# Optimization experiments

Measured on AMD Instinct MI355X. Metric: run time of the kernel, lower is better.

Reference implementation:

```python
import jax, jax.numpy as jnp
import numpy as np

N = 4096
DIM = 128      # dim_in
HID = 256      # mlp hidden_dim
K_IN = 8       # k for linear_k

def _knn_edges(dist, k):
    # dist: [n,n]; k nearest neighbors excluding self (matches heapq loop)
    n = dist.shape[0]
    d = jnp.where(jnp.eye(n, dtype=bool), jnp.inf, dist)
    nbr = jax.lax.top_k(-d, k)[1]                     # [n,k] indices of k smallest
    src = jnp.repeat(jnp.arange(n), k)                # res[0] = i
    dst = nbr.reshape(-1)                             # res[1] = neighbor
    return src, dst

def _gcn_conv(x, src, dst, W, b):
    # torch_geometric GCNConv: add self loops + symmetric normalization
    n = x.shape[0]
    loop = jnp.arange(n)
    s = jnp.concatenate([src, loop])
    t = jnp.concatenate([dst, loop])
    xw = x @ W
    deg = jax.ops.segment_sum(jnp.ones(s.shape[0], x.dtype), t, num_segments=n)
    dinv = jax.lax.rsqrt(deg)                         # deg >= 1 due to self loops
    norm = dinv[s] * dinv[t]
    out = jax.ops.segment_sum(norm[:, None] * xw[s], t, num_segments=n)
    return out + b

def _gcn(x, src, dst, Wg1, bg1, Wg2, bg2):
    h = jax.nn.relu(_gcn_conv(x, src, dst, Wg1, bg1))
    h = _gcn_conv(h, src, dst, Wg2, bg2)              # dropout is identity in eval
    return jax.nn.log_softmax(h, axis=1)

def _conv2d(x, w, b):
    y = jax.lax.conv_general_dilated(x, w, (1, 1), 'SAME',
        dimension_numbers=('NCHW', 'OIHW', 'NCHW'))
    return y + b.reshape(1, -1, 1, 1)

def setup_inputs():
    key = jax.random.key(0)
    ks = jax.random.split(key, 20)
    f32 = jnp.float32
    def w(k, shape):
        fan = shape[0]
        return (jax.random.uniform(k, shape, f32) * 2 - 1) * (1.0 / np.sqrt(fan))
    return {
        'data_x_1': jax.random.normal(ks[0], (1, N, 4), f32),
        'data_x_2': jax.random.normal(ks[1], (1, N, K_IN, 4), f32),
        'Wk': w(ks[2], (K_IN, 1)),        'bk': jnp.zeros((1,), f32),
        'Wg1': w(ks[3], (8, DIM // 2)),   'bg1': jnp.zeros((DIM // 2,), f32),
        'Wg2': w(ks[4], (DIM // 2, DIM)), 'bg2': jnp.zeros((DIM,), f32),
        'Wq': w(ks[5], (3 * DIM, DIM)),   'bq': jnp.zeros((DIM,), f32),
        'Wkey': w(ks[6], (3 * DIM, DIM)), 'bkey': jnp.zeros((DIM,), f32),
        'Woff': w(ks[7], (4, DIM)),       'boff': jnp.zeros((DIM,), f32),
        'pw': jnp.full((1,), 0.25, f32),
        'Wf1': w(ks[8], (DIM, HID)),      'bf1': jnp.zeros((HID,), f32),
        'Wf2': w(ks[9], (HID, HID)),      'bf2': jnp.zeros((HID,), f32),
        'Wf3': w(ks[10], (HID, 4)),       'bf3': jnp.zeros((4,), f32),
        'Wcy3': w(ks[11], (1, 1, 1, 3)),  'bcy3': jnp.zeros((1,), f32),
        'Wcx3': w(ks[12], (1, 1, 3, 1)),  'bcx3': jnp.zeros((1,), f32),
        'Wcy5': w(ks[13], (1, 1, 1, 5)),  'bcy5': jnp.zeros((1,), f32),
        'Wcx5': w(ks[14], (1, 1, 5, 1)),  'bcx5': jnp.zeros((1,), f32),
        'Wcy9': w(ks[15], (1, 1, 1, 9)),  'bcy9': jnp.zeros((1,), f32),
        'Wcx9': w(ks[16], (1, 1, 9, 1)),  'bcx9': jnp.zeros((1,), f32),
    }

def reference(data_x_1, data_x_2, Wk, bk, Wg1, bg1, Wg2, bg2, Wq, bq, Wkey, bkey,
              Woff, boff, pw, Wf1, bf1, Wf2, bf2, Wf3, bf3,
              Wcy3, bcy3, Wcx3, bcx3, Wcy5, bcy5, Wcx5, bcx5, Wcy9, bcy9, Wcx9, bcx9):
    # linear_k over k dimension: [1,n,k,4] -> transpose -> [1,n,4,k] -> [1,n,4]
    dx2 = jnp.swapaxes(data_x_2, 2, 3)
    dx2_out = (dx2 @ Wk + bk)[..., 0]
    data_x = jnp.concatenate([data_x_1, dx2_out], axis=2)   # [1,n,8]
    Ot = data_x[:, :, 4:]                                   # [1,n,4]

    pos = data_x[:, :, 0:2]
    diff = pos[:, :, None, :] - pos[:, None, :, :]          # [1,n,n,2]
    distances = jnp.linalg.norm(diff, axis=3)               # [1,n,n]
    maxd = jnp.max(distances, axis=2, keepdims=True)
    oushi_atte = 1.0 - distances / maxd                     # [1,n,n]

    x0 = data_x[0]
    dist0 = jax.lax.stop_gradient(distances[0])             # knn on detached dist
    embs = []
    for kk in (3, 5, 9):
        src, dst = _knn_edges(dist0, kk)
        embs.append(_gcn(x0, src, dst, Wg1, bg1, Wg2, bg2)[None])
    embedding = jnp.concatenate(embs, axis=2)               # [1,n,3*DIM]

    query = embedding @ Wq + bq                             # [1,n,DIM]
    key_t = embedding @ Wkey + bkey
    scores = jnp.einsum('bnd,bmd->bnm', query, key_t) / jnp.sqrt(jnp.float32(DIM))
    A = scores / jnp.max(scores, axis=2, keepdims=True)     # [1,n,n]

    A4 = A[None]                                            # [1,1,n,n]
    c3 = _conv2d(A4, Wcy3, bcy3) + _conv2d(A4, Wcx3, bcx3)
    c5 = _conv2d(A4, Wcy5, bcy5) + _conv2d(A4, Wcx5, bcx5)
    c9 = _conv2d(A4, Wcy9, bcy9) + _conv2d(A4, Wcx9, bcx9)

    A_cat = jnp.concatenate([A, oushi_atte, c3[0], c5[0], c9[0]], axis=2)  # [1,n,5n]
    A_cat = (A_cat - A_cat.min()) / (A_cat.max() - A_cat.min())

    Ot5 = jnp.tile(Ot, (1, 5, 1))                           # [1,5n,4]
    h = jnp.matmul(A_cat, Ot5)                              # [1,n,4]
    h = h @ Woff + boff                                     # [1,n,DIM]
    h = jnp.where(h > 0, h, pw * h)                         # PReLU (scalar weight)
    h = jax.nn.relu(h @ Wf1 + bf1)
    h = jax.nn.relu(h @ Wf2 + bf2)
    return h @ Wf3 + bf3                                    # [1,n,4]
```

## Files before the change

### kernel.cpp

```cpp
#include <hip/hip_runtime.h>
#include <math.h>

#define NN 4096

typedef __bf16 bf16x8 __attribute__((ext_vector_type(8)));
typedef float  f32x4  __attribute__((ext_vector_type(4)));
typedef _Float16 half4 __attribute__((ext_vector_type(4)));

static __device__ __forceinline__ unsigned enc_f(float f){
    unsigned u = __float_as_uint(f);
    return (u & 0x80000000u) ? ~u : (u | 0x80000000u);
}
static __device__ __forceinline__ float dec_f(unsigned u){
    unsigned b = (u & 0x80000000u) ? (u & 0x7fffffffu) : ~u;
    return __uint_as_float(b);
}
static __device__ __forceinline__ float4 shfl4(float4 v, int src){
    float4 r;
    r.x = __shfl(v.x, src, 64);
    r.y = __shfl(v.y, src, 64);
    r.z = __shfl(v.z, src, 64);
    r.w = __shfl(v.w, src, 64);
    return r;
}
static __device__ __forceinline__ unsigned long long shflx_u64(unsigned long long v, int m){
    unsigned lo = __shfl_xor((unsigned)(v & 0xffffffffu), m, 64);
    unsigned hi = __shfl_xor((unsigned)(v >> 32), m, 64);
    return ((unsigned long long)hi << 32) | lo;
}

__global__ void k_prep(const float* __restrict__ dx1, const float* __restrict__ dx2,
                       const float* __restrict__ Wk, const float* __restrict__ bk,
                       float* __restrict__ x0, float* __restrict__ colsum,
                       float2* __restrict__ pos, float4* __restrict__ otp){
    int n = blockIdx.x*blockDim.x + threadIdx.x;
    if (n >= NN) return;
    float wk[8];
    #pragma unroll
    for (int j=0;j<8;j++) wk[j] = Wk[j];
    float bkv = bk[0];
    float4 d1 = *(const float4*)&dx1[n*4];
    pos[n] = make_float2(d1.x, d1.y);
    #pragma unroll
    for (int c=0;c<4;c++) x0[n*8+c] = (&d1.x)[c];
    float4 ot;
    #pragma unroll
    for (int c=0;c<4;c++){
        float acc = bkv;
        #pragma unroll
        for (int j=0;j<8;j++) acc += dx2[(n*8+j)*4+c]*wk[j];
        x0[n*8+4+c] = acc;
        (&ot.x)[c] = acc;
        atomicAdd(&colsum[c], acc);
    }
    otp[n] = ot;
}

__global__ void k_ty(const float* __restrict__ x0,
        const float* __restrict__ Wcy3, const float* __restrict__ Wcy5, const float* __restrict__ Wcy9,
        float* __restrict__ Ty){
    int j = blockIdx.x*256 + threadIdx.x;
    if (j >= NN) return;
    float Cy[9];
    #pragma unroll
    for (int o=-4;o<=4;o++){
        float c = Wcy9[o+4];
        if (o>=-2 && o<=2) c += Wcy5[o+2];
        if (o>=-1 && o<=1) c += Wcy3[o+1];
        Cy[o+4] = c;
    }
    float4 acc = {0,0,0,0};
    #pragma unroll
    for (int o=-4;o<=4;o++){
        int jj = j - o;
        if ((unsigned)jj < NN){
            float4 ot = *(const float4*)&x0[jj*8+4];
            float c = Cy[o+4];
            acc.x += c*ot.x; acc.y += c*ot.y; acc.z += c*ot.z; acc.w += c*ot.w;
        }
    }
    *(float4*)&Ty[j*4] = acc;
}

#define KCAP 192
__global__ __launch_bounds__(256) void k_dist(const float2* __restrict__ pos,
        const float4* __restrict__ otp,
        float* __restrict__ maxd, int* __restrict__ nbr,
        int* __restrict__ cnt3, int* __restrict__ cnt5, int* __restrict__ cnt9,
        float* __restrict__ dOt){
    __shared__ unsigned long long cbuf[4][KCAP];
    int tid = threadIdx.x;
    int w = tid >> 6, lane = tid & 63;
    int i = blockIdx.x*4 + w;
    float2 pi = pos[i];

    float lmax = 0.f, lmin = INFINITY;
    float4 dacc = {0,0,0,0};
    for (int t=0;t<64;t++){
        int j = (t<<6) | lane;
        float2 p = pos[j];
        float dx = pi.x - p.x, dy = pi.y - p.y;
        float d = sqrtf(dx*dx + dy*dy);
        lmax = fmaxf(lmax, d);
        float4 otj = otp[j];
        dacc.x += d*otj.x; dacc.y += d*otj.y; dacc.z += d*otj.z; dacc.w += d*otj.w;
        if (j != i) lmin = fminf(lmin, d);
    }
    #pragma unroll
    for (int m=1;m<64;m<<=1){
        lmax = fmaxf(lmax, __shfl_xor(lmax, m, 64));
        dacc.x += __shfl_xor(dacc.x, m, 64);
        dacc.y += __shfl_xor(dacc.y, m, 64);
        dacc.z += __shfl_xor(dacc.z, m, 64);
        dacc.w += __shfl_xor(dacc.w, m, 64);
    }
    if (lane==0){
        maxd[i] = lmax;
        *(float4*)&dOt[i*4] = dacc;
    }
    float v = lmin, T = 0.f;
    #pragma unroll
    for (int r=0;r<9;r++){
        float m = v;
        #pragma unroll
        for (int s=1;s<64;s<<=1) m = fminf(m, __shfl_xor(m, s, 64));
        T = m;
        if (v == m) v = INFINITY;
    }

    int base = 0;
    for (int t=0;t<64;t++){
        int j = (t<<6) | lane;
        float2 p = pos[j];
        float dx = pi.x - p.x, dy = pi.y - p.y;
        float d = sqrtf(dx*dx + dy*dy);
        bool pass = (j != i) && (d <= T);
        unsigned long long b = __ballot(pass);
        if (b){
            int pre = __popcll(b & ((1ull<<lane)-1ull));
            int idx = base + pre;
            if (pass && idx < KCAP)
                cbuf[w][idx] = ((unsigned long long)__float_as_uint(d) << 32) | (unsigned)j;
            base += __popcll(b);
        }
    }
    int M = base < KCAP ? base : KCAP;

    unsigned long long c0 = (lane      < M) ? cbuf[w][lane]      : ~0ULL;
    unsigned long long c1 = (lane+64   < M) ? cbuf[w][lane+64]   : ~0ULL;
    unsigned long long c2 = (lane+128  < M) ? cbuf[w][lane+128]  : ~0ULL;
    for (int r=0;r<9;r++){
        unsigned long long mv = c0 < c1 ? c0 : c1;
        mv = mv < c2 ? mv : c2;
        #pragma unroll
        for (int s=1;s<64;s<<=1){
            unsigned long long o = shflx_u64(mv, s);
            if (o < mv) mv = o;
        }
        if (c0 == mv) c0 = ~0ULL;
        else if (c1 == mv) c1 = ~0ULL;
        else if (c2 == mv) c2 = ~0ULL;
        if (lane == 0){
            int j = (int)(mv & 0xffffffffu);
            nbr[i*9+r] = j;
            atomicAdd(&cnt9[j], 1);
            if (r<5) atomicAdd(&cnt5[j], 1);
            if (r<3) atomicAdd(&cnt3[j], 1);
        }
    }
}

__global__ __launch_bounds__(256) void k_scan(const int* __restrict__ cnt3,
        const int* __restrict__ cnt5, const int* __restrict__ cnt9,
        int* __restrict__ offc, float* __restrict__ dinvc){
    __shared__ int part[256];
    int tid = threadIdx.x;
    for (int g=0; g<3; g++){
        const int* cp = g==0?cnt3:(g==1?cnt5:cnt9);
        int base = tid*16;
        int loc[16]; int s=0;
        #pragma unroll
        for (int q=0;q<16;q++){ loc[q]=s; s += cp[base+q]; }
        part[tid]=s; __syncthreads();
        for (int d=1; d<256; d<<=1){
            int v = (tid>=d) ? part[tid-d] : 0;
            __syncthreads();
            part[tid] += v;
            __syncthreads();
        }
        int pre = (tid==0) ? 0 : part[tid-1];
        #pragma unroll
        for (int q=0;q<16;q++){
            offc[g*NN + base + q]  = pre + loc[q];
            dinvc[g*NN + base + q] = rsqrtf((float)cp[base+q] + 1.f);
        }
        __syncthreads();
    }
}

__global__ void k_fill(const int* __restrict__ nbr, const int* __restrict__ offc,
        int* __restrict__ cur, int* __restrict__ rev){
    int i = blockIdx.x*256 + threadIdx.x;
    if (i >= NN) return;
    #pragma unroll
    for (int t=0;t<9;t++){
        int j = nbr[i*9+t];
        int gmin = t<3 ? 0 : (t<5 ? 1 : 2);
        for (int g=gmin; g<3; g++){
            int pos = atomicAdd(&cur[g*NN+j], 1);
            int rb = (g==0) ? 0 : (g==1 ? NN*3 : NN*8);
            rev[rb + offc[g*NN+j] + pos] = i;
        }
    }
}

__global__ void k_y1(const float* __restrict__ x0, const float* __restrict__ Wg1,
                     float* __restrict__ xw){
    int idx = blockIdx.x*256 + threadIdx.x;
    if (idx >= NN*64) return;
    int n = idx>>6, c = idx&63;
    float acc = 0.f;
    #pragma unroll
    for (int k=0;k<8;k++) acc += x0[n*8+k]*Wg1[k*64+c];
    xw[idx] = acc;
}

__global__ __launch_bounds__(256) void k_h1y2(const float* __restrict__ xw,
        const int* __restrict__ offc,
        const int* __restrict__ cnt3, const int* __restrict__ cnt5, const int* __restrict__ cnt9,
        const int* __restrict__ rev, const float* __restrict__ dinvc,
        const float* __restrict__ bg1, const float* __restrict__ Wg2,
        float* __restrict__ y2){
    __shared__ float h1s[12][64];
    int n0 = blockIdx.x*4, tid = threadIdx.x;
    for (int s=tid; s<768; s+=256){
        int p = s>>6, k = s&63, g = p>>2, n = n0+(p&3);
        const int* cp = g==0?cnt3:(g==1?cnt5:cnt9);
        int rb = (g==0) ? 0 : (g==1 ? NN*3 : NN*8);
        int cnt = cp[n];
        int o = rb + offc[g*NN+n];
        float dv = dinvc[g*NN+n];
        float srow = dv*xw[n*64+k];
        for (int e=0;e<cnt;e++){
            int i = rev[o+e];
            srow += dinvc[g*NN+i]*xw[i*64+k];
        }
        float v = dv*srow + bg1[k];
        h1s[p][k] = v>0.f ? v : 0.f;
    }
    __syncthreads();
    int c = tid & 127, ph = tid>>7;
    float a6[6] = {0,0,0,0,0,0};
    for (int k=0;k<64;k++){
        float w = Wg2[k*128+c];
        #pragma unroll
        for (int q=0;q<6;q++) a6[q] += h1s[q*2+ph][k]*w;
    }
    #pragma unroll
    for (int q=0;q<6;q++){
        int p = q*2+ph, g = p>>2, n = n0+(p&3);
        float dv = dinvc[g*NN+n];
        y2[(size_t)g*NN*128 + (size_t)n*128 + c] = dv*a6[q];
    }
}

__global__ __launch_bounds__(128) void k_fin(const float* __restrict__ y2,
        const int* __restrict__ offc,
        const int* __restrict__ cnt3, const int* __restrict__ cnt5, const int* __restrict__ cnt9,
        const int* __restrict__ rev, const float* __restrict__ dinvc,
        const float* __restrict__ bg2, float* __restrict__ emb){
    __shared__ float sm[2], ss[2];
    int b = blockIdx.x;
    int n = b & (NN-1), g = b >> 12;
    const int* cp = g==0?cnt3:(g==1?cnt5:cnt9);
    int rb = (g==0) ? 0 : (g==1 ? NN*3 : NN*8);
    int cnt = cp[n];
    int o = rb + offc[g*NN+n];
    float dv = dinvc[g*NN+n];
    int c = threadIdx.x;
    const float* yg = y2 + (size_t)g*NN*128;
    float s = yg[(size_t)n*128 + c];
    for (int e=0;e<cnt;e++){
        int i = rev[o+e];
        s += yg[(size_t)i*128 + c];
    }
    float v = dv*s + bg2[c];
    float m = v;
    #pragma unroll
    for (int st=1;st<64;st<<=1) m = fmaxf(m, __shfl_xor(m, st, 64));
    if ((c&63)==0) sm[c>>6] = m;
    __syncthreads();
    m = fmaxf(sm[0], sm[1]);
    float e = expf(v - m);
    float t = e;
    #pragma unroll
    for (int st=1;st<64;st<<=1) t += __shfl_xor(t, st, 64);
    if ((c&63)==0) ss[c>>6] = t;
    __syncthreads();
    t = ss[0]+ss[1];
    emb[n*384 + g*128 + c] = v - m - logf(t);
}

__global__ __launch_bounds__(256) void k_qk(const float* __restrict__ emb,
        const float* __restrict__ Wq, const float* __restrict__ bq,
        const float* __restrict__ Wkey, const float* __restrict__ bkey,
        __bf16* __restrict__ qh, __bf16* __restrict__ ql,
        __bf16* __restrict__ kh, __bf16* __restrict__ kl){
    __shared__ float es[8][384];
    int n0 = blockIdx.x*8;
    int tid = threadIdx.x;
    for (int idx=tid; idx<8*384; idx+=256){
        int m = idx/384, k = idx%384;
        es[m][k] = emb[(n0+m)*384+k];
    }
    __syncthreads();
    int c = tid & 127;
    int sel = tid >> 7;
    const float* W = sel ? Wkey : Wq;
    float b = sel ? bkey[c] : bq[c];
    float acc[8];
    #pragma unroll
    for (int m=0;m<8;m++) acc[m]=b;
    for (int k=0;k<384;k++){
        float w = W[k*128+c];
        #pragma unroll
        for (int m=0;m<8;m++) acc[m] += es[m][k]*w;
    }
    __bf16* oh = sel ? kh : qh;
    __bf16* ol = sel ? kl : ql;
    #pragma unroll
    for (int m=0;m<8;m++){
        float v = acc[m];
        __bf16 h = (__bf16)v;
        oh[(size_t)(n0+m)*128+c] = h;
        ol[(size_t)(n0+m)*128+c] = (__bf16)(v - (float)h);
    }
}

__global__ __launch_bounds__(256) void k_scores(
        const __bf16* __restrict__ qh, const __bf16* __restrict__ ql,
        const __bf16* __restrict__ kh, const __bf16* __restrict__ kl,
        _Float16* __restrict__ scores,
        unsigned* __restrict__ rowmaxenc, unsigned* __restrict__ rowminenc){
    __shared__ float tl[4][16][68];
    int bx = blockIdx.x & 31;
    int by = blockIdx.x >> 5;
    int tid = threadIdx.x;
    int w = tid >> 6, lane = tid & 63;
    int li = lane & 15, g = lane >> 4;
    int r0 = by*128 + (w>>1)*64;
    int c0 = bx*128 + (w&1)*64;

    f32x4 acc[4][4] = {};
    for (int ks=0; ks<4; ++ks){
        int kofs = ks*32 + g*8;
        bf16x8 ah[4], al[4], bh[4], bl[4];
        #pragma unroll
        for (int f=0; f<4; ++f){
            ah[f] = *(const bf16x8*)&qh[(size_t)(r0+f*16+li)*128 + kofs];
            al[f] = *(const bf16x8*)&ql[(size_t)(r0+f*16+li)*128 + kofs];
            bh[f] = *(const bf16x8*)&kh[(size_t)(c0+f*16+li)*128 + kofs];
            bl[f] = *(const bf16x8*)&kl[(size_t)(c0+f*16+li)*128 + kofs];
        }
        #pragma unroll
        for (int fr=0; fr<4; ++fr){
            #pragma unroll
            for (int fc=0; fc<4; ++fc){
                acc[fr][fc] = __builtin_amdgcn_mfma_f32_16x16x32_bf16(ah[fr], bh[fc], acc[fr][fc], 0, 0, 0);
                acc[fr][fc] = __builtin_amdgcn_mfma_f32_16x16x32_bf16(ah[fr], bl[fc], acc[fr][fc], 0, 0, 0);
                acc[fr][fc] = __builtin_amdgcn_mfma_f32_16x16x32_bf16(al[fr], bh[fc], acc[fr][fc], 0, 0, 0);
            }
        }
    }
    #pragma unroll
    for (int fr=0; fr<4; ++fr){
        #pragma unroll
        for (int r=0; r<4; ++r){
            int row = r0 + fr*16 + g*4 + r;
            float mx = -INFINITY, mn = INFINITY;
            #pragma unroll
            for (int fc=0; fc<4; ++fc){
                float v = acc[fr][fc][r];
                mx = fmaxf(mx, v);
                mn = fminf(mn, v);
            }
            #pragma unroll
            for (int s=1; s<16; s<<=1){
                mx = fmaxf(mx, __shfl_xor(mx, s, 64));
                mn = fminf(mn, __shfl_xor(mn, s, 64));
            }
            if (li == 0){
                atomicMax(&rowmaxenc[row], enc_f(mx));
                atomicMin(&rowminenc[row], enc_f(mn));
            }
        }
    }
    for (int fr=0; fr<4; ++fr){
        #pragma unroll
        for (int fc=0; fc<4; ++fc)
            #pragma unroll
            for (int r=0; r<4; ++r)
                tl[w][g*4+r][fc*16+li] = acc[fr][fc][r];
        __syncthreads();
        #pragma unroll
        for (int q=0; q<4; ++q){
            int row = q*4 + g;
            float4 v;
            v.x = tl[w][row][li*4+0];
            v.y = tl[w][row][li*4+1];
            v.z = tl[w][row][li*4+2];
            v.w = tl[w][row][li*4+3];
            half4 hv = { (_Float16)v.x, (_Float16)v.y, (_Float16)v.z, (_Float16)v.w };
            *(half4*)&scores[(size_t)(r0+fr*16+row)*NN + c0 + li*4] = hv;
        }
        __syncthreads();
    }
}

__global__ void k_invr(const unsigned* __restrict__ rowmaxenc, float* __restrict__ invr){
    int i = blockIdx.x*256 + threadIdx.x;
    if (i >= NN) return;
    invr[i] = 1.f/dec_f(rowmaxenc[i]);
}

__global__ __launch_bounds__(256) void k_cconv(const _Float16* __restrict__ scores,
        const float* __restrict__ invr,
        const float* __restrict__ Wcy3, const float* __restrict__ Wcx3,
        const float* __restrict__ Wcy5, const float* __restrict__ Wcx5,
        const float* __restrict__ Wcy9, const float* __restrict__ Wcx9,
        const float* __restrict__ bcy3, const float* __restrict__ bcx3,
        const float* __restrict__ bcy5, const float* __restrict__ bcx5,
        const float* __restrict__ bcy9, const float* __restrict__ bcx9,
        float* __restrict__ mnmx){
    __shared__ float smn[4], smx[4];
    int tid = threadIdx.x;
    int w = tid >> 6, lane = tid & 63;
    int strip = blockIdx.x;
    int i0 = (blockIdx.y*4 + w)*19;
    int colbase = strip*248 - 4 + lane*4;
    bool lv = (colbase >= 0) && (colbase + 3 < NN);
    bool outLane = (lane >= 1) && (lane < 63) && lv;

    float wy3[3],wx3[3],wy5[5],wx5[5],wy9[9],wx9[9];
    #pragma unroll
    for (int t=0;t<3;t++){ wy3[t]=Wcy3[t]; wx3[t]=Wcx3[t]; }
    #pragma unroll
    for (int t=0;t<5;t++){ wy5[t]=Wcy5[t]; wx5[t]=Wcx5[t]; }
    #pragma unroll
    for (int t=0;t<9;t++){ wy9[t]=Wcy9[t]; wx9[t]=Wcx9[t]; }
    float bc3 = bcy3[0]+bcx3[0];
    float bc5 = bcy5[0]+bcx5[0];
    float bc9 = bcy9[0]+bcx9[0];

    float4 win[9];
    float mn = INFINITY, mx = -INFINITY;
    const int laneL = lane - 1, laneR = lane + 1;

    for (int tb = 0; tb < 3; ++tb){
        #pragma unroll
        for (int u = 0; u < 9; ++u){
            int t  = tb*9 + u;
            int ri = i0 - 4 + t;
            float4 a = make_float4(0,0,0,0);
            if (((unsigned)ri < NN) && lv){
                float iv = invr[ri];
                half4 hv = *(const half4*)&scores[(size_t)ri*NN + colbase];
                a.x = (float)hv.x*iv; a.y = (float)hv.y*iv;
                a.z = (float)hv.z*iv; a.w = (float)hv.w*iv;
            }
            win[u] = a;
            int ro = i0 + t - 8;
            if (t >= 8 && ro < NN){
                float4 ctr = win[(u+5)%9];
                float4 wl = shfl4(ctr, laneL);
                float4 wr = shfl4(ctr, laneR);
                if (outLane){
                    float cw[12] = {wl.x,wl.y,wl.z,wl.w, ctr.x,ctr.y,ctr.z,ctr.w, wr.x,wr.y,wr.z,wr.w};
                    #pragma unroll
                    for (int c=0;c<4;c++){
                        float cx9 = ((win[(u+1)%9][c]*wx9[0] + win[(u+2)%9][c]*wx9[1]) + (win[(u+3)%9][c]*wx9[2] + win[(u+4)%9][c]*wx9[3]))
                                  + ((win[(u+5)%9][c]*wx9[4] + win[(u+6)%9][c]*wx9[5]) + (win[(u+7)%9][c]*wx9[6] + win[(u+8)%9][c]*wx9[7]))
                                  + win[u][c]*wx9[8];
                        float cx5 = ((win[(u+3)%9][c]*wx5[0] + win[(u+4)%9][c]*wx5[1]) + (win[(u+5)%9][c]*wx5[2] + win[(u+6)%9][c]*wx5[3]))
                                  + win[(u+7)%9][c]*wx5[4];
                        float cx3 = (win[(u+4)%9][c]*wx3[0] + win[(u+5)%9][c]*wx3[1]) + win[(u+6)%9][c]*wx3[2];
                        float cy9 = ((cw[c+0]*wy9[0] + cw[c+1]*wy9[1]) + (cw[c+2]*wy9[2] + cw[c+3]*wy9[3]))
                                  + ((cw[c+4]*wy9[4] + cw[c+5]*wy9[5]) + (cw[c+6]*wy9[6] + cw[c+7]*wy9[7]))
                                  + cw[c+8]*wy9[8];
                        float cy5 = ((cw[c+2]*wy5[0] + cw[c+3]*wy5[1]) + (cw[c+4]*wy5[2] + cw[c+5]*wy5[3]))
                                  + cw[c+6]*wy5[4];
                        float cy3 = (cw[c+3]*wy3[0] + cw[c+4]*wy3[1]) + cw[c+5]*wy3[2];
                        float c3v = cy3+cx3+bc3, c5v = cy5+cx5+bc5, c9v = cy9+cx9+bc9;
                        mn = fminf(mn, fminf(fminf(c3v,c5v),c9v));
                        mx = fmaxf(mx, fmaxf(fmaxf(c3v,c5v),c9v));
                    }
                }
            }
        }
    }
    #pragma unroll
    for (int m=1; m<64; m<<=1){
        mn = fminf(mn, __shfl_xor(mn, m, 64));
        mx = fmaxf(mx, __shfl_xor(mx, m, 64));
    }
    if (lane == 0){ smn[w] = mn; smx[w] = mx; }
    __syncthreads();
    if (tid == 0){
        float a0 = fminf(fminf(smn[0],smn[1]), fminf(smn[2],smn[3]));
        float b0 = fmaxf(fmaxf(smx[0],smx[1]), fmaxf(smx[2],smx[3]));
        int bid = blockIdx.y*gridDim.x + blockIdx.x;
        mnmx[bid] = a0;
        mnmx[1024 + bid] = b0;
    }
}

__global__ __launch_bounds__(256) void k_kot(const __bf16* __restrict__ kh, const __bf16* __restrict__ kl,
        const float* __restrict__ x0, const float* __restrict__ Ty,
        float* __restrict__ kOt){
    __shared__ float red[256][8];
    int d = blockIdx.x, tid = threadIdx.x;
    float a[8] = {0,0,0,0,0,0,0,0};
    for (int j = tid; j < NN; j += 256){
        float kv = (float)kh[(size_t)j*128 + d] + (float)kl[(size_t)j*128 + d];
        float4 ot = *(const float4*)&x0[j*8+4];
        float4 ty = *(const float4*)&Ty[j*4];
        a[0] += kv*ot.x; a[1] += kv*ot.y; a[2] += kv*ot.z; a[3] += kv*ot.w;
        a[4] += kv*ty.x; a[5] += kv*ty.y; a[6] += kv*ty.z; a[7] += kv*ty.w;
    }
    #pragma unroll
    for (int q=0;q<8;q++) red[tid][q] = a[q];
    __syncthreads();
    for (int s=128; s>0; s>>=1){
        if (tid < s){
            #pragma unroll
            for (int q=0;q<8;q++) red[tid][q] += red[tid+s][q];
        }
        __syncthreads();
    }
    if (tid < 8) kOt[d*8 + tid] = red[0][tid];
}

__global__ __launch_bounds__(256) void k_asd(
        const __bf16* __restrict__ qh, const __bf16* __restrict__ ql,
        const float* __restrict__ kOt,
        const unsigned* __restrict__ rowmaxenc, const float* __restrict__ maxd,
        const float* __restrict__ dOt, const float* __restrict__ colsum,
        const float* __restrict__ bcy3, const float* __restrict__ bcx3,
        const float* __restrict__ bcy5, const float* __restrict__ bcx5,
        const float* __restrict__ bcy9, const float* __restrict__ bcx9,
        float* __restrict__ ASdot, float* __restrict__ Bv){
    __shared__ float kst[128*8];
    int tid = threadIdx.x;
    for (int s = tid; s < 1024; s += 256) kst[s] = kOt[s];
    __syncthreads();
    int lane = tid & 63, r = tid >> 6;
    int i = blockIdx.x*4 + r;
    float a[8] = {0,0,0,0,0,0,0,0};
    #pragma unroll
    for (int dd=0; dd<2; ++dd){
        int d = lane + dd*64;
        float qv = (float)qh[(size_t)i*128 + d] + (float)ql[(size_t)i*128 + d];
        #pragma unroll
        for (int q=0;q<8;q++) a[q] += qv * kst[d*8+q];
    }
    #pragma unroll
    for (int m=1; m<64; m<<=1){
        #pragma unroll
        for (int q=0;q<8;q++) a[q] += __shfl_xor(a[q], m, 64);
    }
    if (lane == 0){
        float iv = 1.f/dec_f(rowmaxenc[i]);
        float imv = 1.f/maxd[i];
        float bcsum = bcy3[0]+bcx3[0]+bcy5[0]+bcx5[0]+bcy9[0]+bcx9[0];
        float k = 1.f + bcsum;
        float4 cs = *(const float4*)colsum;
        float4 dv = *(const float4*)&dOt[i*4];
        float4 pa = {iv*a[0], iv*a[1], iv*a[2], iv*a[3]};
        float4 b;
        b.x = cs.x*k - imv*dv.x + iv*a[4];
        b.y = cs.y*k - imv*dv.y + iv*a[5];
        b.z = cs.z*k - imv*dv.z + iv*a[6];
        b.w = cs.w*k - imv*dv.w + iv*a[7];
        *(float4*)&ASdot[i*4] = pa;
        *(float4*)&Bv[i*4]    = b;
    }
}

__global__ __launch_bounds__(256) void k_gmm(const float* __restrict__ mnmx,
        const unsigned* __restrict__ rowminenc, const unsigned* __restrict__ rowmaxenc,
        float* __restrict__ gmm){
    __shared__ float smn[256], smx[256];
    int tid = threadIdx.x;
    float mn = 0.f, mx = 1.f;
    for (int i=tid; i<NN; i+=256){
        float rmx = dec_f(rowmaxenc[i]);
        float q = dec_f(rowminenc[i]) / rmx;
        mn = fminf(mn, fminf(1.f, q));
        mx = fmaxf(mx, fmaxf(1.f, q));
    }
    for (int b=tid; b<918; b+=256){
        mn = fminf(mn, mnmx[b]);
        mx = fmaxf(mx, mnmx[1024+b]);
    }
    smn[tid]=mn; smx[tid]=mx; __syncthreads();
    for (int s=128;s>0;s>>=1){
        if (tid<s){ smn[tid]=fminf(smn[tid],smn[tid+s]); smx[tid]=fmaxf(smx[tid],smx[tid+s]); }
        __syncthreads();
    }
    if (tid==0){ gmm[0]=smn[0]; gmm[1]=smx[0]; }
}

__global__ void k_hfin(const float* __restrict__ ASdot, const float* __restrict__ Bv,
        const float* __restrict__ Wcx3, const float* __restrict__ Wcx5, const float* __restrict__ Wcx9,
        const float* __restrict__ gmm, const float* __restrict__ colsum,
        float* __restrict__ hfin){
    int i = blockIdx.x*256 + threadIdx.x;
    if (i >= NN) return;
    float Cx[9];
    #pragma unroll
    for (int o=-4;o<=4;o++){
        float c = Wcx9[o+4];
        if (o>=-2 && o<=2) c += Wcx5[o+2];
        if (o>=-1 && o<=1) c += Wcx3[o+1];
        Cx[o+4] = c;
    }
    float4 h = *(const float4*)&Bv[i*4];
    float4 a0 = *(const float4*)&ASdot[i*4];
    h.x += a0.x; h.y += a0.y; h.z += a0.z; h.w += a0.w;
    #pragma unroll
    for (int o=-4;o<=4;o++){
        int r = i + o;
        if ((unsigned)r < NN){
            float4 av = *(const float4*)&ASdot[r*4];
            float c = Cx[o+4];
            h.x += c*av.x; h.y += c*av.y; h.z += c*av.z; h.w += c*av.w;
        }
    }
    float mnv = gmm[0], mxv = gmm[1];
    float s = 1.f/(mxv-mnv), oa = -mnv*s;
    float4 cs = *(const float4*)colsum;
    float4 out;
    out.x = s*h.x + 5.f*oa*cs.x;
    out.y = s*h.y + 5.f*oa*cs.y;
    out.z = s*h.z + 5.f*oa*cs.z;
    out.w = s*h.w + 5.f*oa*cs.w;
    *(float4*)&hfin[i*4] = out;
}

__global__ __launch_bounds__(256) void k_mlp(const float* __restrict__ hfin,
        const float* __restrict__ Woff, const float* __restrict__ boff, const float* __restrict__ pw,
        const float* __restrict__ Wf1, const float* __restrict__ bf1,
        const float* __restrict__ Wf2, const float* __restrict__ bf2,
        const float* __restrict__ Wf3, const float* __restrict__ bf3,
        float* __restrict__ out){
    __shared__ float h1[8][128];
    __shared__ float h2[8][256];
    __shared__ float h3[8][256];
    int n0 = blockIdx.x*8, tid = threadIdx.x;
    float p = pw[0];
    {
        int c = tid & 127, mb = (tid>>7)*4;
        #pragma unroll
        for (int mm=0; mm<4; mm++){
            int m = mb+mm;
            float v = boff[c];
            #pragma unroll
            for (int k=0;k<4;k++) v += hfin[(n0+m)*4+k]*Woff[k*128+c];
            h1[m][c] = v>0.f ? v : p*v;
        }
    }
    __syncthreads();
    {
        int c = tid;
        float acc[8];
        #pragma unroll
        for (int m=0;m<8;m++) acc[m] = bf1[c];
        for (int k=0;k<128;k++){
            float w = Wf1[k*256+c];
            #pragma unroll
            for (int m=0;m<8;m++) acc[m] += h1[m][k]*w;
        }
        #pragma unroll
        for (int m=0;m<8;m++) h2[m][c] = acc[m]>0.f?acc[m]:0.f;
    }
    __syncthreads();
    {
        int c = tid;
        float acc[8];
        #pragma unroll
        for (int m=0;m<8;m++) acc[m] = bf2[c];
        for (int k=0;k<256;k++){
            float w = Wf2[k*256+c];
            #pragma unroll
            for (int m=0;m<8;m++) acc[m] += h2[m][k]*w;
        }
        #pragma unroll
        for (int m=0;m<8;m++) h3[m][c] = acc[m]>0.f?acc[m]:0.f;
    }
    __syncthreads();
    int w = tid >> 6, lane = tid & 63;
    #pragma unroll
    for (int mm=0; mm<2; ++mm){
        int m = w*2 + mm;
        float4 acc = {0,0,0,0};
        #pragma unroll
        for (int q=0;q<4;q++){
            int k = lane + q*64;
            float hv = h3[m][k];
            float4 w3 = *(const float4*)&Wf3[k*4];
            acc.x += hv*w3.x; acc.y += hv*w3.y; acc.z += hv*w3.z; acc.w += hv*w3.w;
        }
        #pragma unroll
        for (int s=1; s<64; s<<=1){
            acc.x += __shfl_xor(acc.x, s, 64);
            acc.y += __shfl_xor(acc.y, s, 64);
            acc.z += __shfl_xor(acc.z, s, 64);
            acc.w += __shfl_xor(acc.w, s, 64);
        }
        if (lane == 0){
            float4 o;
            o.x = acc.x + bf3[0]; o.y = acc.y + bf3[1];
            o.z = acc.z + bf3[2]; o.w = acc.w + bf3[3];
            *(float4*)&out[(n0+m)*4] = o;
        }
    }
}

extern "C" void kernel_launch(void* const* d_in, const int* in_sizes, int n_in,
                              void* d_out, int out_size, void* d_ws, size_t ws_size,
                              hipStream_t stream){
    const float* dx1  = (const float*)d_in[0];
    const float* dx2  = (const float*)d_in[1];
    const float* Wk   = (const float*)d_in[2];
    const float* bk   = (const float*)d_in[3];
    const float* Wg1  = (const float*)d_in[4];
    const float* bg1  = (const float*)d_in[5];
    const float* Wg2  = (const float*)d_in[6];
    const float* bg2  = (const float*)d_in[7];
    const float* Wq   = (const float*)d_in[8];
    const float* bq   = (const float*)d_in[9];
    const float* Wkey = (const float*)d_in[10];
    const float* bkey = (const float*)d_in[11];
    const float* Woff = (const float*)d_in[12];
    const float* boff = (const float*)d_in[13];
    const float* pw   = (const float*)d_in[14];
    const float* Wf1  = (const float*)d_in[15];
    const float* bf1  = (const float*)d_in[16];
    const float* Wf2  = (const float*)d_in[17];
    const float* bf2  = (const float*)d_in[18];
    const float* Wf3  = (const float*)d_in[19];
    const float* bf3  = (const float*)d_in[20];
    const float* Wcy3 = (const float*)d_in[21];
    const float* bcy3 = (const float*)d_in[22];
    const float* Wcx3 = (const float*)d_in[23];
    const float* bcx3 = (const float*)d_in[24];
    const float* Wcy5 = (const float*)d_in[25];
    const float* bcy5 = (const float*)d_in[26];
    const float* Wcx5 = (const float*)d_in[27];
    const float* bcx5 = (const float*)d_in[28];
    const float* Wcy9 = (const float*)d_in[29];
    const float* bcy9 = (const float*)d_in[30];
    const float* Wcx9 = (const float*)d_in[31];
    const float* bcx9 = (const float*)d_in[32];

    char* ws = (char*)d_ws;
    size_t off = 0;
    auto alloc = [&](size_t b)->void*{ void* p = ws + off; off += (b + 255) & ~(size_t)255; return p; };

    char* zbase = ws + off;
    float*    colsum    = (float*)   alloc(4*4);
    int*      cnt3      = (int*)     alloc((size_t)NN*4);
    int*      cnt5      = (int*)     alloc((size_t)NN*4);
    int*      cnt9      = (int*)     alloc((size_t)NN*4);
    int*      cur       = (int*)     alloc((size_t)3*NN*4);
    unsigned* rowmaxenc = (unsigned*)alloc((size_t)NN*4);
    size_t zbytes = (size_t)((ws + off) - zbase);
    unsigned* rowminenc = (unsigned*)alloc((size_t)NN*4);

    float*  x0    = (float*) alloc((size_t)NN*8*4);
    float2* pos   = (float2*)alloc((size_t)NN*8);
    float4* otp   = (float4*)alloc((size_t)NN*16);
    float*  maxd  = (float*) alloc((size_t)NN*4);
    int*    nbr   = (int*)   alloc((size_t)NN*9*4);
    int*    offc  = (int*)   alloc((size_t)3*NN*4);
    float*  dinvc = (float*) alloc((size_t)3*NN*4);
    int*    rev   = (int*)   alloc((size_t)NN*17*4);
    float*  xw    = (float*) alloc((size_t)NN*64*4);
    float*  y2    = (float*) alloc((size_t)3*NN*128*4);
    float*  emb   = (float*) alloc((size_t)NN*384*4);
    __bf16* qh    = (__bf16*)alloc((size_t)NN*128*2);
    __bf16* ql    = (__bf16*)alloc((size_t)NN*128*2);
    __bf16* kh    = (__bf16*)alloc((size_t)NN*128*2);
    __bf16* kl    = (__bf16*)alloc((size_t)NN*128*2);
    _Float16* scores = (_Float16*)alloc((size_t)NN*NN*2);
    float* Tyb    = (float*)alloc((size_t)NN*4*4);
    float* invr   = (float*)alloc((size_t)NN*4);
    float* dOt    = (float*)alloc((size_t)NN*4*4);
    float* kOt    = (float*)alloc((size_t)128*8*4);
    float* ASd    = (float*)alloc((size_t)NN*4*4);
    float* Bv     = (float*)alloc((size_t)NN*4*4);
    float* mnmx   = (float*)alloc((size_t)2*1024*4);
    float* gmm    = (float*)alloc(2*4);
    float* hfin   = (float*)alloc((size_t)NN*4*4);
    (void)ws_size; (void)in_sizes; (void)n_in; (void)out_size;

    hipMemsetAsync(zbase, 0, zbytes, stream);
    hipMemsetAsync(rowminenc, 0xFF, (size_t)NN*4, stream);

    k_prep<<<16,256,0,stream>>>(dx1,dx2,Wk,bk,x0,colsum,pos,otp);
    k_ty  <<<16,256,0,stream>>>(x0,Wcy3,Wcy5,Wcy9,Tyb);
    k_dist<<<NN/4,256,0,stream>>>(pos,otp,maxd,nbr,cnt3,cnt5,cnt9,dOt);
    k_scan<<<1,256,0,stream>>>(cnt3,cnt5,cnt9,offc,dinvc);
    k_fill<<<16,256,0,stream>>>(nbr,offc,cur,rev);

    k_y1  <<<NN*64/256,256,0,stream>>>(x0,Wg1,xw);
    k_h1y2<<<NN/4,256,0,stream>>>(xw,offc,cnt3,cnt5,cnt9,rev,dinvc,bg1,Wg2,y2);
    k_fin <<<NN*3,128,0,stream>>>(y2,offc,cnt3,cnt5,cnt9,rev,dinvc,bg2,emb);

    k_qk<<<NN/8,256,0,stream>>>(emb,Wq,bq,Wkey,bkey,qh,ql,kh,kl);
    k_scores<<<1024,256,0,stream>>>(qh,ql,kh,kl,scores,rowmaxenc,rowminenc);
    k_invr<<<16,256,0,stream>>>(rowmaxenc,invr);
    k_kot<<<128,256,0,stream>>>(kh,kl,x0,Tyb,kOt);

    k_cconv<<<dim3(17,54),256,0,stream>>>(scores,invr,
        Wcy3,Wcx3,Wcy5,Wcx5,Wcy9,Wcx9,
        bcy3,bcx3,bcy5,bcx5,bcy9,bcx9, mnmx);
    k_asd<<<NN/4,256,0,stream>>>(qh,ql,kOt,rowmaxenc,maxd,dOt,colsum,
        bcy3,bcx3,bcy5,bcx5,bcy9,bcx9, ASd, Bv);
    k_gmm<<<1,256,0,stream>>>(mnmx,rowminenc,rowmaxenc,gmm);
    k_hfin<<<16,256,0,stream>>>(ASd,Bv,Wcx3,Wcx5,Wcx9,gmm,colsum,hfin);
    k_mlp<<<NN/8,256,0,stream>>>(hfin,Woff,boff,pw,Wf1,bf1,Wf2,bf2,Wf3,bf3,(float*)d_out);
}
```

Measured before the change: 302.8 us.

## Move row max/min out of scores GEMM into separate reduction pass, narrow tile

The scores kernel no longer does per-row max/min reductions with global atomics on encoded floats. A new k_rowmm kernel re-reads the fp16 score matrix, reduces each row with one wavefront, and writes rowmax, rowmin and the inverse row max as plain floats. The scores tile is narrowed from 128x128 to 128x64 per block, which doubles the block count. This removes atomic contention, a memset and the encode/decode steps, but adds a full extra read of the 32 MB score matrix and reduces operand reuse in the GEMM. Row extrema now come from fp16-rounded values rather than fp32 accumulators, which slightly changes numerics.

```diff
diff --git a/kernel.cpp b/kernel.cpp
--- a/kernel.cpp
+++ b/kernel.cpp
@@ -7,14 +7,6 @@
 typedef float  f32x4  __attribute__((ext_vector_type(4)));
 typedef _Float16 half4 __attribute__((ext_vector_type(4)));
 
-static __device__ __forceinline__ unsigned enc_f(float f){
-    unsigned u = __float_as_uint(f);
-    return (u & 0x80000000u) ? ~u : (u | 0x80000000u);
-}
-static __device__ __forceinline__ float dec_f(unsigned u){
-    unsigned b = (u & 0x80000000u) ? (u & 0x7fffffffu) : ~u;
-    return __uint_as_float(b);
-}
 static __device__ __forceinline__ float4 shfl4(float4 v, int src){
     float4 r;
     r.x = __shfl(v.x, src, 64);
@@ -340,87 +332,86 @@
 __global__ __launch_bounds__(256) void k_scores(
         const __bf16* __restrict__ qh, const __bf16* __restrict__ ql,
         const __bf16* __restrict__ kh, const __bf16* __restrict__ kl,
-        _Float16* __restrict__ scores,
-        unsigned* __restrict__ rowmaxenc, unsigned* __restrict__ rowminenc){
-    __shared__ float tl[4][16][68];
-    int bx = blockIdx.x & 31;
-    int by = blockIdx.x >> 5;
+        _Float16* __restrict__ scores){
+    __shared__ float tl[4][16][36];
+    int bx = blockIdx.x & 63;
+    int by = blockIdx.x >> 6;
     int tid = threadIdx.x;
     int w = tid >> 6, lane = tid & 63;
     int li = lane & 15, g = lane >> 4;
     int r0 = by*128 + (w>>1)*64;
-    int c0 = bx*128 + (w&1)*64;
-
-    f32x4 acc[4][4] = {};
+    int c0 = bx*64  + (w&1)*32;
+
+    f32x4 acc[4][2] = {};
     for (int ks=0; ks<4; ++ks){
         int kofs = ks*32 + g*8;
-        bf16x8 ah[4], al[4], bh[4], bl[4];
+        bf16x8 ah[4], al[4], bh[2], bl[2];
         #pragma unroll
         for (int f=0; f<4; ++f){
             ah[f] = *(const bf16x8*)&qh[(size_t)(r0+f*16+li)*128 + kofs];
             al[f] = *(const bf16x8*)&ql[(size_t)(r0+f*16+li)*128 + kofs];
+        }
+        #pragma unroll
+        for (int f=0; f<2; ++f){
             bh[f] = *(const bf16x8*)&kh[(size_t)(c0+f*16+li)*128 + kofs];
             bl[f] = *(const bf16x8*)&kl[(size_t)(c0+f*16+li)*128 + kofs];
         }
         #pragma unroll
         for (int fr=0; fr<4; ++fr){
             #pragma unroll
-            for (int fc=0; fc<4; ++fc){
+            for (int fc=0; fc<2; ++fc){
                 acc[fr][fc] = __builtin_amdgcn_mfma_f32_16x16x32_bf16(ah[fr], bh[fc], acc[fr][fc], 0, 0, 0);
                 acc[fr][fc] = __builtin_amdgcn_mfma_f32_16x16x32_bf16(ah[fr], bl[fc], acc[fr][fc], 0, 0, 0);
                 acc[fr][fc] = __builtin_amdgcn_mfma_f32_16x16x32_bf16(al[fr], bh[fc], acc[fr][fc], 0, 0, 0);
             }
         }
     }
-    #pragma unroll
     for (int fr=0; fr<4; ++fr){
         #pragma unroll
-        for (int r=0; r<4; ++r){
-            int row = r0 + fr*16 + g*4 + r;
-            float mx = -INFINITY, mn = INFINITY;
-            #pragma unroll
-            for (int fc=0; fc<4; ++fc){
-                float v = acc[fr][fc][r];
-                mx = fmaxf(mx, v);
-                mn = fminf(mn, v);
-            }
-            #pragma unroll
-            for (int s=1; s<16; s<<=1){
-                mx = fmaxf(mx, __shfl_xor(mx, s, 64));
-                mn = fminf(mn, __shfl_xor(mn, s, 64));
-            }
-            if (li == 0){
-                atomicMax(&rowmaxenc[row], enc_f(mx));
-                atomicMin(&rowminenc[row], enc_f(mn));
-            }
-        }
-    }
-    for (int fr=0; fr<4; ++fr){
-        #pragma unroll
-        for (int fc=0; fc<4; ++fc)
+        for (int fc=0; fc<2; ++fc)
             #pragma unroll
             for (int r=0; r<4; ++r)
                 tl[w][g*4+r][fc*16+li] = acc[fr][fc][r];
         __syncthreads();
         #pragma unroll
-        for (int q=0; q<4; ++q){
-            int row = q*4 + g;
+        for (int q=0; q<2; ++q){
+            int row = q*8 + (lane>>3);
+            int c4 = (lane&7)*4;
             float4 v;
-            v.x = tl[w][row][li*4+0];
-            v.y = tl[w][row][li*4+1];
-            v.z = tl[w][row][li*4+2];
-            v.w = tl[w][row][li*4+3];
+            v.x = tl[w][row][c4+0];
+            v.y = tl[w][row][c4+1];
+            v.z = tl[w][row][c4+2];
+            v.w = tl[w][row][c4+3];
             half4 hv = { (_Float16)v.x, (_Float16)v.y, (_Float16)v.z, (_Float16)v.w };
-            *(half4*)&scores[(size_t)(r0+fr*16+row)*NN + c0 + li*4] = hv;
+            *(half4*)&scores[(size_t)(r0+fr*16+row)*NN + c0 + c4] = hv;
         }
         __syncthreads();
     }
 }
 
-__global__ void k_invr(const unsigned* __restrict__ rowmaxenc, float* __restrict__ invr){
-    int i = blockIdx.x*256 + threadIdx.x;
-    if (i >= NN) return;
-    invr[i] = 1.f/dec_f(rowmaxenc[i]);
+__global__ __launch_bounds__(256) void k_rowmm(const _Float16* __restrict__ scores,
+        float* __restrict__ rowmax, float* __restrict__ rowmin, float* __restrict__ invr){
+    int tid = threadIdx.x;
+    int w = tid >> 6, lane = tid & 63;
+    int i = blockIdx.x*4 + w;
+    const _Float16* row = scores + (size_t)i*NN;
+    float mx = -INFINITY, mn = INFINITY;
+    for (int t=0; t<16; ++t){
+        half4 hv = *(const half4*)&row[(t*64+lane)*4];
+        float a = (float)hv.x, b = (float)hv.y, c = (float)hv.z, d = (float)hv.w;
+        mx = fmaxf(mx, fmaxf(fmaxf(a,b), fmaxf(c,d)));
+        mn = fminf(mn, fminf(fminf(a,b), fminf(c,d)));
+    }
+    #pragma unroll
+    for (int s=1; s<64; s<<=1){
+        mx = fmaxf(mx, __shfl_xor(mx, s, 64));
+        mn = fminf(mn, __shfl_xor(mn, s, 64));
+    }
+    if (lane == 0){
+        rowmax[i] = mx;
+        rowmin[i] = mn;
+        invr[i] = 1.f/mx;
+    }
 }
 
 __global__ __launch_bounds__(256) void k_cconv(const _Float16* __restrict__ scores,
@@ -543,7 +534,7 @@
 __global__ __launch_bounds__(256) void k_asd(
         const __bf16* __restrict__ qh, const __bf16* __restrict__ ql,
         const float* __restrict__ kOt,
-        const unsigned* __restrict__ rowmaxenc, const float* __restrict__ maxd,
+        const float* __restrict__ invr, const float* __restrict__ maxd,
         const float* __restrict__ dOt, const float* __restrict__ colsum,
         const float* __restrict__ bcy3, const float* __restrict__ bcx3,
         const float* __restrict__ bcy5, const float* __restrict__ bcx5,
@@ -569,7 +560,7 @@
         for (int q=0;q<8;q++) a[q] += __shfl_xor(a[q], m, 64);
     }
     if (lane == 0){
-        float iv = 1.f/dec_f(rowmaxenc[i]);
+        float iv = invr[i];
         float imv = 1.f/maxd[i];
         float bcsum = bcy3[0]+bcx3[0]+bcy5[0]+bcx5[0]+bcy9[0]+bcx9[0];
         float k = 1.f + bcsum;
@@ -587,14 +578,13 @@
 }
 
 __global__ __launch_bounds__(256) void k_gmm(const float* __restrict__ mnmx,
-        const unsigned* __restrict__ rowminenc, const unsigned* __restrict__ rowmaxenc,
+        const float* __restrict__ rowmin, const float* __restrict__ rowmax,
         float* __restrict__ gmm){
     __shared__ float smn[256], smx[256];
     int tid = threadIdx.x;
     float mn = 0.f, mx = 1.f;
     for (int i=tid; i<NN; i+=256){
-        float rmx = dec_f(rowmaxenc[i]);
-        float q = dec_f(rowminenc[i]) / rmx;
+        float q = rowmin[i] / rowmax[i];
         mn = fminf(mn, fminf(1.f, q));
         mx = fmaxf(mx, fmaxf(1.f, q));
     }
@@ -773,9 +763,7 @@
     int*      cnt5      = (int*)     alloc((size_t)NN*4);
     int*      cnt9      = (int*)     alloc((size_t)NN*4);
     int*      cur       = (int*)     alloc((size_t)3*NN*4);
-    unsigned* rowmaxenc = (unsigned*)alloc((size_t)NN*4);
     size_t zbytes = (size_t)((ws + off) - zbase);
-    unsigned* rowminenc = (unsigned*)alloc((size_t)NN*4);
 
     float*  x0    = (float*) alloc((size_t)NN*8*4);
     float2* pos   = (float2*)alloc((size_t)NN*8);
@@ -794,6 +782,8 @@
     __bf16* kl    = (__bf16*)alloc((size_t)NN*128*2);
     _Float16* scores = (_Float16*)alloc((size_t)NN*NN*2);
     float* Tyb    = (float*)alloc((size_t)NN*4*4);
+    float* rowmax = (float*)alloc((size_t)NN*4);
+    float* rowmin = (float*)alloc((size_t)NN*4);
     float* invr   = (float*)alloc((size_t)NN*4);
     float* dOt    = (float*)alloc((size_t)NN*4*4);
     float* kOt    = (float*)alloc((size_t)128*8*4);
@@ -805,7 +795,6 @@
     (void)ws_size; (void)in_sizes; (void)n_in; (void)out_size;
 
     hipMemsetAsync(zbase, 0, zbytes, stream);
-    hipMemsetAsync(rowminenc, 0xFF, (size_t)NN*4, stream);
 
     k_prep<<<16,256,0,stream>>>(dx1,dx2,Wk,bk,x0,colsum,pos,otp);
     k_ty  <<<16,256,0,stream>>>(x0,Wcy3,Wcy5,Wcy9,Tyb);
@@ -818,16 +807,16 @@
     k_fin <<<NN*3,128,0,stream>>>(y2,offc,cnt3,cnt5,cnt9,rev,dinvc,bg2,emb);
 
     k_qk<<<NN/8,256,0,stream>>>(emb,Wq,bq,Wkey,bkey,qh,ql,kh,kl);
-    k_scores<<<1024,256,0,stream>>>(qh,ql,kh,kl,scores,rowmaxenc,rowminenc);
-    k_invr<<<16,256,0,stream>>>(rowmaxenc,invr);
+    k_scores<<<2048,256,0,stream>>>(qh,ql,kh,kl,scores);
+    k_rowmm<<<NN/4,256,0,stream>>>(scores,rowmax,rowmin,invr);
     k_kot<<<128,256,0,stream>>>(kh,kl,x0,Tyb,kOt);
 
     k_cconv<<<dim3(17,54),256,0,stream>>>(scores,invr,
         Wcy3,Wcx3,Wcy5,Wcx5,Wcy9,Wcx9,
         bcy3,bcx3,bcy5,bcx5,bcy9,bcx9, mnmx);
-    k_asd<<<NN/4,256,0,stream>>>(qh,ql,kOt,rowmaxenc,maxd,dOt,colsum,
+    k_asd<<<NN/4,256,0,stream>>>(qh,ql,kOt,invr,maxd,dOt,colsum,
         bcy3,bcx3,bcy5,bcx5,bcy9,bcx9, ASd, Bv);
-    k_gmm<<<1,256,0,stream>>>(mnmx,rowminenc,rowmaxenc,gmm);
+    k_gmm<<<1,256,0,stream>>>(mnmx,rowmin,rowmax,gmm);
     k_hfin<<<16,256,0,stream>>>(ASd,Bv,Wcx3,Wcx5,Wcx9,gmm,colsum,hfin);
     k_mlp<<<NN/8,256,0,stream>>>(hfin,Woff,boff,pw,Wf1,bf1,Wf2,bf2,Wf3,bf3,(float*)d_out);
 }
```

Measured after the change: 304.2 us. Within noise of the previous version (+0.5%).
